# Kernel tuning notes

Hardware: AMD Instinct MI355X
Metric: run time of the kernel (lower is better)

The kernel has to match this reference:

```python
import jax, jax.numpy as jnp
import numpy as np

D_IN = 1024
D_OUT = 1024


def setup_inputs() -> dict:
    key = jax.random.key(0)
    kx, kq, kk, kv = jax.random.split(key, 4)
    x = jax.random.normal(kx, (4, 2048, D_IN), dtype=jnp.float32)
    # nn.Linear weight has shape [d_out, d_in]; y = x @ W.T
    s = 1.0 / np.sqrt(D_IN)
    W_query = jax.random.uniform(kq, (D_OUT, D_IN), jnp.float32, -s, s)
    W_key = jax.random.uniform(kk, (D_OUT, D_IN), jnp.float32, -s, s)
    W_value = jax.random.uniform(kv, (D_OUT, D_IN), jnp.float32, -s, s)
    return {"x": x, "W_query": W_query, "W_key": W_key, "W_value": W_value}


def reference(x, W_query, W_key, W_value):
    # x: [b, n, d_in]; W_*: [d_out, d_in]
    q = jnp.einsum("bnd,kd->bnk", x, W_query)
    k = jnp.einsum("bnd,kd->bnk", x, W_key)
    v = jnp.einsum("bnd,kd->bnk", x, W_value)
    d_k = W_query.shape[0]
    scores = jnp.einsum("bqk,bnk->bqn", q, k) * (d_k ** -0.5)  # [b, n, n]
    weights = jax.nn.softmax(scores, axis=-1)
    return jnp.einsum("bqn,bnk->bqk", weights, v)
```

## Files before the change

### kernel.cpp

```cpp
#include <hip/hip_runtime.h>
#include <hip/hip_bf16.h>
#include <stdint.h>


typedef __attribute__((ext_vector_type(8))) short bf16x8;
typedef __attribute__((ext_vector_type(4))) float f32x4;

__device__ __forceinline__ void async_copy16(const void* g, void* l) {
  __builtin_amdgcn_global_load_lds(
      (__attribute__((address_space(1))) void*)(g),
      (__attribute__((address_space(3))) void*)(l),
      16, 0, 0);
}

__global__ __launch_bounds__(256)
void gemm_qkv(const __hip_bfloat16* __restrict__ A,
              const __hip_bfloat16* __restrict__ B,
              __hip_bfloat16* __restrict__ Q,
              __hip_bfloat16* __restrict__ Kk,
              __hip_bfloat16* __restrict__ Vt)
{
  __shared__ __align__(16) __hip_bfloat16 As[128 * 64];
  __shared__ __align__(16) __hip_bfloat16 Bs[128 * 64];

  const int K = 1024;
  const long long tile_m = (long long)blockIdx.y * 128;
  const long long tile_n = (long long)blockIdx.x * 128;

  const int tid  = threadIdx.x;
  const int wid  = tid >> 6;
  const int lane = tid & 63;

  const int srow = wid * 8 + (lane >> 3);
  const int scol = (((lane & 7) ^ (lane >> 3))) * 8;

  const __hip_bfloat16* aptr = A + (tile_m + srow) * K + scol;
  const __hip_bfloat16* bptr = B + (tile_n + srow) * K + scol;
  char* la = (char*)As + (wid * 8) * 128;
  char* lb = (char*)Bs + (wid * 8) * 128;

  const int wm   = (wid >> 1) * 64;
  const int wn   = (wid & 1) * 64;
  const int quad = lane >> 4;
  const int l16  = lane & 15;
  const int sw   = l16 & 7;

  const bf16x8* Asv = (const bf16x8*)As;
  const bf16x8* Bsv = (const bf16x8*)Bs;

  f32x4 acc[4][4];
  #pragma unroll
  for (int mi = 0; mi < 4; ++mi)
    #pragma unroll
    for (int ni = 0; ni < 4; ++ni)
      acc[mi][ni] = (f32x4){0.f, 0.f, 0.f, 0.f};

  for (int k0 = 0; k0 < K; k0 += 64) {
    #pragma unroll
    for (int p = 0; p < 4; ++p) {
      async_copy16(aptr + (long long)p * 32 * K, la + p * 32 * 128);
      async_copy16(bptr + (long long)p * 32 * K, lb + p * 32 * 128);
    }
    aptr += 64;
    bptr += 64;
    __syncthreads();

    #pragma unroll
    for (int kk = 0; kk < 2; ++kk) {
      bf16x8 af[4], bfr[4];
      const int ch = (kk * 4 + quad);
      #pragma unroll
      for (int mi = 0; mi < 4; ++mi) af[mi]  = Asv[(wm + mi * 16 + l16) * 8 + (ch ^ sw)];
      #pragma unroll
      for (int ni = 0; ni < 4; ++ni) bfr[ni] = Bsv[(wn + ni * 16 + l16) * 8 + (ch ^ sw)];
      #pragma unroll
      for (int mi = 0; mi < 4; ++mi)
        #pragma unroll
        for (int ni = 0; ni < 4; ++ni)
          acc[mi][ni] = __builtin_amdgcn_mfma_f32_16x16x32_bf16(af[mi], bfr[ni], acc[mi][ni], 0, 0, 0);
    }
    __syncthreads();
  }

  const int mat = (int)(tile_n >> 10);
  if (mat < 2) {
    __hip_bfloat16* outp = (mat == 0) ? Q : Kk;
    const float scale = (mat == 0) ? 0.03125f : 1.0f;
    const int coln0 = (int)(tile_n & 1023);
    #pragma unroll
    for (int mi = 0; mi < 4; ++mi) {
      #pragma unroll
      for (int r = 0; r < 4; ++r) {
        const long long row = tile_m + wm + mi * 16 + quad * 4 + r;
        #pragma unroll
        for (int ni = 0; ni < 4; ++ni) {
          const int col = coln0 + wn + ni * 16 + l16;
          outp[row * 1024 + col] = __float2bfloat16(acc[mi][ni][r] * scale);
        }
      }
    }
  } else {
    const int b    = (int)(tile_m >> 11);
    const int seq0 = (int)(tile_m & 2047);
    const int d0   = (int)(tile_n - 2048);
    #pragma unroll
    for (int mi = 0; mi < 4; ++mi) {
      const int seq = seq0 + wm + mi * 16 + quad * 4;
      #pragma unroll
      for (int ni = 0; ni < 4; ++ni) {
        const int d = d0 + wn + ni * 16 + l16;
        union { ushort4 u; unsigned short s[4]; } pk;
        #pragma unroll
        for (int r = 0; r < 4; ++r)
          pk.s[r] = __bfloat16_as_ushort(__float2bfloat16(acc[mi][ni][r]));
        *(ushort4*)(Vt + ((long long)(b * 1024 + d)) * 2048 + seq) = pk.u;
      }
    }
  }
}

__global__ __launch_bounds__(256)
void gemm_s_exp(const __hip_bfloat16* __restrict__ A,
                const __hip_bfloat16* __restrict__ B,
                __hip_bfloat16* __restrict__ Cout,
                float* __restrict__ part)
{
  __shared__ __align__(16) __hip_bfloat16 As[128 * 64];
  __shared__ __align__(16) __hip_bfloat16 Bs[128 * 64];

  const int K = 1024, N = 2048;
  const int bz = blockIdx.z;
  A += (long long)bz * 2048 * 1024;
  B += (long long)bz * 2048 * 1024;

  const long long tile_m = (long long)blockIdx.y * 128;
  const long long tile_n = (long long)blockIdx.x * 128;

  const int tid  = threadIdx.x;
  const int wid  = tid >> 6;
  const int lane = tid & 63;

  const int srow = wid * 8 + (lane >> 3);
  const int scol = (((lane & 7) ^ (lane >> 3))) * 8;

  const __hip_bfloat16* aptr = A + (tile_m + srow) * K + scol;
  const __hip_bfloat16* bptr = B + (tile_n + srow) * K + scol;
  char* la = (char*)As + (wid * 8) * 128;
  char* lb = (char*)Bs + (wid * 8) * 128;

  const int wm   = (wid >> 1) * 64;
  const int wn   = (wid & 1) * 64;
  const int quad = lane >> 4;
  const int l16  = lane & 15;
  const int sw   = l16 & 7;

  const bf16x8* Asv = (const bf16x8*)As;
  const bf16x8* Bsv = (const bf16x8*)Bs;

  f32x4 acc[4][4];
  #pragma unroll
  for (int mi = 0; mi < 4; ++mi)
    #pragma unroll
    for (int ni = 0; ni < 4; ++ni)
      acc[mi][ni] = (f32x4){0.f, 0.f, 0.f, 0.f};

  for (int k0 = 0; k0 < K; k0 += 64) {
    #pragma unroll
    for (int p = 0; p < 4; ++p) {
      async_copy16(aptr + (long long)p * 32 * K, la + p * 32 * 128);
      async_copy16(bptr + (long long)p * 32 * K, lb + p * 32 * 128);
    }
    aptr += 64;
    bptr += 64;
    __syncthreads();

    #pragma unroll
    for (int kk = 0; kk < 2; ++kk) {
      bf16x8 af[4], bfr[4];
      const int ch = (kk * 4 + quad);
      #pragma unroll
      for (int mi = 0; mi < 4; ++mi) af[mi]  = Asv[(wm + mi * 16 + l16) * 8 + (ch ^ sw)];
      #pragma unroll
      for (int ni = 0; ni < 4; ++ni) bfr[ni] = Bsv[(wn + ni * 16 + l16) * 8 + (ch ^ sw)];
      #pragma unroll
      for (int mi = 0; mi < 4; ++mi)
        #pragma unroll
        for (int ni = 0; ni < 4; ++ni)
          acc[mi][ni] = __builtin_amdgcn_mfma_f32_16x16x32_bf16(af[mi], bfr[ni], acc[mi][ni], 0, 0, 0);
    }
    __syncthreads();
  }

  __hip_bfloat16* C = Cout + (long long)bz * 2048 * 2048;
  #pragma unroll
  for (int mi = 0; mi < 4; ++mi) {
    #pragma unroll
    for (int r = 0; r < 4; ++r) {
      const long long row = tile_m + wm + mi * 16 + quad * 4 + r;
      float s = 0.f;
      #pragma unroll
      for (int ni = 0; ni < 4; ++ni) {
        const float e = __expf(acc[mi][ni][r]);
        const __hip_bfloat16 h = __float2bfloat16(e);
        C[row * N + tile_n + wn + ni * 16 + l16] = h;
        s += __bfloat162float(h);
      }
      #pragma unroll
      for (int off = 1; off < 16; off <<= 1) s += __shfl_xor(s, off, 64);
      if (l16 == 0)
        part[((long long)bz * 2048 + row) * 32 + blockIdx.x * 2 + (wid & 1)] = s;
    }
  }
}

__global__ __launch_bounds__(256)
void gemm_pv(const __hip_bfloat16* __restrict__ A,
             const __hip_bfloat16* __restrict__ B,
             const float* __restrict__ part,
             float* __restrict__ Cout)
{
  __shared__ __align__(16) __hip_bfloat16 As[128 * 64];
  __shared__ __align__(16) __hip_bfloat16 Bs[64 * 64];
  __shared__ float rinv[128];

  const int K = 2048, N = 1024;
  const int bz = blockIdx.z;
  A += (long long)bz * 2048 * 2048;
  B += (long long)bz * 1024 * 2048;

  const long long tile_m = (long long)blockIdx.y * 128;
  const long long tile_n = (long long)blockIdx.x * 64;

  const int tid  = threadIdx.x;
  const int wid  = tid >> 6;
  const int lane = tid & 63;

  const int srow = wid * 8 + (lane >> 3);
  const int scol = (((lane & 7) ^ (lane >> 3))) * 8;

  const __hip_bfloat16* aptr = A + (tile_m + srow) * K + scol;
  const __hip_bfloat16* bptr = B + (tile_n + srow) * K + scol;
  char* la = (char*)As + (wid * 8) * 128;
  char* lb = (char*)Bs + (wid * 8) * 128;

  const int wm   = (wid >> 1) * 64;
  const int wn   = (wid & 1) * 32;
  const int quad = lane >> 4;
  const int l16  = lane & 15;
  const int sw   = l16 & 7;

  const bf16x8* Asv = (const bf16x8*)As;
  const bf16x8* Bsv = (const bf16x8*)Bs;

  f32x4 acc[4][2];
  #pragma unroll
  for (int mi = 0; mi < 4; ++mi)
    #pragma unroll
    for (int ni = 0; ni < 2; ++ni)
      acc[mi][ni] = (f32x4){0.f, 0.f, 0.f, 0.f};

  for (int k0 = 0; k0 < K; k0 += 64) {
    #pragma unroll
    for (int p = 0; p < 4; ++p)
      async_copy16(aptr + (long long)p * 32 * K, la + p * 32 * 128);
    #pragma unroll
    for (int p = 0; p < 2; ++p)
      async_copy16(bptr + (long long)p * 32 * K, lb + p * 32 * 128);
    aptr += 64;
    bptr += 64;
    __syncthreads();

    #pragma unroll
    for (int kk = 0; kk < 2; ++kk) {
      bf16x8 af[4], bfr[2];
      const int ch = (kk * 4 + quad);
      #pragma unroll
      for (int mi = 0; mi < 4; ++mi) af[mi]  = Asv[(wm + mi * 16 + l16) * 8 + (ch ^ sw)];
      #pragma unroll
      for (int ni = 0; ni < 2; ++ni) bfr[ni] = Bsv[(wn + ni * 16 + l16) * 8 + (ch ^ sw)];
      #pragma unroll
      for (int mi = 0; mi < 4; ++mi)
        #pragma unroll
        for (int ni = 0; ni < 2; ++ni)
          acc[mi][ni] = __builtin_amdgcn_mfma_f32_16x16x32_bf16(af[mi], bfr[ni], acc[mi][ni], 0, 0, 0);
    }
    __syncthreads();
  }

  if (tid < 128) {
    const float4* pp = (const float4*)(part + ((long long)bz * 2048 + tile_m + tid) * 32);
    float s = 0.f;
    #pragma unroll
    for (int j = 0; j < 8; ++j) {
      const float4 f = pp[j];
      s += f.x + f.y + f.z + f.w;
    }
    rinv[tid] = 1.f / s;
  }
  __syncthreads();

  float* C = Cout + (long long)bz * 2048 * 1024;
  #pragma unroll
  for (int mi = 0; mi < 4; ++mi) {
    #pragma unroll
    for (int r = 0; r < 4; ++r) {
      const int rloc = wm + mi * 16 + quad * 4 + r;
      const float inv = rinv[rloc];
      const long long row = tile_m + rloc;
      #pragma unroll
      for (int ni = 0; ni < 2; ++ni) {
        const long long col = tile_n + wn + ni * 16 + l16;
        C[row * N + col] = acc[mi][ni][r] * inv;
      }
    }
  }
}

__global__ __launch_bounds__(256)
void cast_all(const float* __restrict__ x,
              const float* __restrict__ Wq, const float* __restrict__ Wk,
              const float* __restrict__ Wv,
              __hip_bfloat16* __restrict__ xb, __hip_bfloat16* __restrict__ wcat)
{
  const int bx = blockIdx.x;
  const float* src;
  __hip_bfloat16* dst;
  int i;
  if (bx < 8192) {
    src = x; dst = xb; i = bx * 256 + threadIdx.x;
  } else {
    const int which = (bx - 8192) >> 10;
    src = (which == 0) ? Wq : (which == 1) ? Wk : Wv;
    dst = wcat + (long long)which * 1048576;
    i = ((bx - 8192) & 1023) * 256 + threadIdx.x;
  }
  const float4 f = ((const float4*)src)[i];
  union { ushort4 u; __hip_bfloat16 h[4]; } r;
  r.h[0] = __float2bfloat16(f.x);
  r.h[1] = __float2bfloat16(f.y);
  r.h[2] = __float2bfloat16(f.z);
  r.h[3] = __float2bfloat16(f.w);
  ((ushort4*)dst)[i] = r.u;
}

extern "C" void kernel_launch(void* const* d_in, const int* in_sizes, int n_in,
                              void* d_out, int out_size, void* d_ws, size_t ws_size,
                              hipStream_t stream)
{
  (void)in_sizes; (void)n_in; (void)out_size; (void)ws_size;

  const float* x  = (const float*)d_in[0];
  const float* Wq = (const float*)d_in[1];
  const float* Wk = (const float*)d_in[2];
  const float* Wv = (const float*)d_in[3];
  float* out = (float*)d_out;

  char* ws = (char*)d_ws;
  __hip_bfloat16* xb   = (__hip_bfloat16*)(ws);
  float*          part = (float*)(ws);
  __hip_bfloat16* wcat = (__hip_bfloat16*)(ws + (16LL << 20));
  __hip_bfloat16* Q    = (__hip_bfloat16*)(ws + (22LL << 20));
  __hip_bfloat16* Kk   = (__hip_bfloat16*)(ws + (38LL << 20));
  __hip_bfloat16* Vt   = (__hip_bfloat16*)(ws + (54LL << 20));
  __hip_bfloat16* S    = (__hip_bfloat16*)(ws + (70LL << 20));

  cast_all<<<11264, 256, 0, stream>>>(x, Wq, Wk, Wv, xb, wcat);

  gemm_qkv<<<dim3(24, 64, 1), 256, 0, stream>>>(xb, wcat, Q, Kk, Vt);

  gemm_s_exp<<<dim3(16, 16, 4), 256, 0, stream>>>(Q, Kk, S, part);

  gemm_pv<<<dim3(16, 16, 4), 256, 0, stream>>>(S, Vt, part, out);
}
```

Baseline: 250.5 us.

## Fuse cast and three GEMMs into one persistent kernel with grid barriers

Replaces the four separate launches (cast, QKV projection, scores+exp, PV) with one persistent 1024-block kernel. Each phase becomes a device function, and software grid barriers built on atomic counters separate the phases. The aim is to remove the launch gaps and tail idle time between kernels. In exchange it relies on all 1024 blocks being co-resident, caps registers through launch_bounds(256,4), and keeps the barrier counters in the tail of the output buffer; a wrong guess about residency could deadlock, and the register cap could cause spills.

```diff
diff --git a/kernel.cpp b/kernel.cpp
--- a/kernel.cpp
+++ b/kernel.cpp
@@ -13,19 +13,63 @@
       16, 0, 0);
 }
 
-__global__ __launch_bounds__(256)
-void gemm_qkv(const __hip_bfloat16* __restrict__ A,
-              const __hip_bfloat16* __restrict__ B,
-              __hip_bfloat16* __restrict__ Q,
-              __hip_bfloat16* __restrict__ Kk,
-              __hip_bfloat16* __restrict__ Vt)
-{
-  __shared__ __align__(16) __hip_bfloat16 As[128 * 64];
-  __shared__ __align__(16) __hip_bfloat16 Bs[128 * 64];
+__device__ __forceinline__ void grid_barrier(unsigned* cnt, unsigned target) {
+  __syncthreads();
+  if (threadIdx.x == 0) {
+    __threadfence();
+    atomicAdd(cnt, 1u);
+    while (__hip_atomic_load(cnt, __ATOMIC_RELAXED, __HIP_MEMORY_SCOPE_AGENT) < target)
+      __builtin_amdgcn_s_sleep(32);
+    __threadfence();
+  }
+  __syncthreads();
+}
+
+
+__device__ __forceinline__ void phase_cast(
+    const float* __restrict__ x,
+    const float* __restrict__ Wq, const float* __restrict__ Wk,
+    const float* __restrict__ Wv,
+    __hip_bfloat16* __restrict__ xb, __hip_bfloat16* __restrict__ wcat)
+{
+  for (int i = blockIdx.x * 256 + threadIdx.x; i < 2883584; i += 1024 * 256) {
+    const float* src;
+    __hip_bfloat16* dst;
+    int j;
+    if (i < 2097152) {
+      src = x; dst = xb; j = i;
+    } else {
+      const int k = i - 2097152;
+      const int which = k >> 18;
+      src = (which == 0) ? Wq : (which == 1) ? Wk : Wv;
+      dst = wcat + (long long)which * 1048576;
+      j = k & 262143;
+    }
+    const float4 f = ((const float4*)src)[j];
+    union { ushort4 u; __hip_bfloat16 h[4]; } r;
+    r.h[0] = __float2bfloat16(f.x);
+    r.h[1] = __float2bfloat16(f.y);
+    r.h[2] = __float2bfloat16(f.z);
+    r.h[3] = __float2bfloat16(f.w);
+    ((ushort4*)dst)[j] = r.u;
+  }
+}
+
+__device__ __forceinline__ void qkv_tile(
+    char* smem,
+    const __hip_bfloat16* __restrict__ A,
+    const __hip_bfloat16* __restrict__ B,
+    __hip_bfloat16* __restrict__ Q,
+    __hip_bfloat16* __restrict__ Kk,
+    __hip_bfloat16* __restrict__ Vt,
+    int ty, int tx)
+{
+  __hip_bfloat16* As = (__hip_bfloat16*)smem;
+  __hip_bfloat16* Bs = (__hip_bfloat16*)(smem + 16384);
 
   const int K = 1024;
-  const long long tile_m = (long long)blockIdx.y * 128;
-  const long long tile_n = (long long)blockIdx.x * 128;
+  const long long tile_m = (long long)ty * 128;
+  const long long tile_n = (long long)tx * 128;
 
   const int tid  = threadIdx.x;
   const int wid  = tid >> 6;
@@ -119,22 +163,23 @@
   }
 }
 
-__global__ __launch_bounds__(256)
-void gemm_s_exp(const __hip_bfloat16* __restrict__ A,
-                const __hip_bfloat16* __restrict__ B,
-                __hip_bfloat16* __restrict__ Cout,
-                float* __restrict__ part)
-{
-  __shared__ __align__(16) __hip_bfloat16 As[128 * 64];
-  __shared__ __align__(16) __hip_bfloat16 Bs[128 * 64];
+__device__ __forceinline__ void s_exp_tile(
+    char* smem,
+    const __hip_bfloat16* __restrict__ Qg,
+    const __hip_bfloat16* __restrict__ Kg,
+    __hip_bfloat16* __restrict__ Sg,
+    float* __restrict__ part,
+    int bz, int ty, int tx)
+{
+  __hip_bfloat16* As = (__hip_bfloat16*)smem;
+  __hip_bfloat16* Bs = (__hip_bfloat16*)(smem + 16384);
 
   const int K = 1024, N = 2048;
-  const int bz = blockIdx.z;
-  A += (long long)bz * 2048 * 1024;
-  B += (long long)bz * 2048 * 1024;
-
-  const long long tile_m = (long long)blockIdx.y * 128;
-  const long long tile_n = (long long)blockIdx.x * 128;
+  const __hip_bfloat16* A = Qg + (long long)bz * 2048 * 1024;
+  const __hip_bfloat16* B = Kg + (long long)bz * 2048 * 1024;
+
+  const long long tile_m = (long long)ty * 128;
+  const long long tile_n = (long long)tx * 128;
 
   const int tid  = threadIdx.x;
   const int wid  = tid >> 6;
@@ -191,7 +236,7 @@
     __syncthreads();
   }
 
-  __hip_bfloat16* C = Cout + (long long)bz * 2048 * 2048;
+  __hip_bfloat16* C = Sg + (long long)bz * 2048 * 2048;
   #pragma unroll
   for (int mi = 0; mi < 4; ++mi) {
     #pragma unroll
@@ -208,28 +253,29 @@
       #pragma unroll
       for (int off = 1; off < 16; off <<= 1) s += __shfl_xor(s, off, 64);
       if (l16 == 0)
-        part[((long long)bz * 2048 + row) * 32 + blockIdx.x * 2 + (wid & 1)] = s;
-    }
-  }
-}
-
-__global__ __launch_bounds__(256)
-void gemm_pv(const __hip_bfloat16* __restrict__ A,
-             const __hip_bfloat16* __restrict__ B,
-             const float* __restrict__ part,
-             float* __restrict__ Cout)
-{
-  __shared__ __align__(16) __hip_bfloat16 As[128 * 64];
-  __shared__ __align__(16) __hip_bfloat16 Bs[64 * 64];
-  __shared__ float rinv[128];
+        part[((long long)bz * 2048 + row) * 32 + tx * 2 + (wid & 1)] = s;
+    }
+  }
+}
+
+__device__ __forceinline__ void pv_tile(
+    char* smem,
+    const __hip_bfloat16* __restrict__ Sg,
+    const __hip_bfloat16* __restrict__ Vtg,
+    const float* __restrict__ part,
+    float* __restrict__ Cout,
+    int bz, int ty, int tx)
+{
+  __hip_bfloat16* As = (__hip_bfloat16*)smem;
+  __hip_bfloat16* Bs = (__hip_bfloat16*)(smem + 16384);
+  float* rinv = (float*)(smem + 24576);
 
   const int K = 2048, N = 1024;
-  const int bz = blockIdx.z;
-  A += (long long)bz * 2048 * 2048;
-  B += (long long)bz * 1024 * 2048;
-
-  const long long tile_m = (long long)blockIdx.y * 128;
-  const long long tile_n = (long long)blockIdx.x * 64;
+  const __hip_bfloat16* A = Sg  + (long long)bz * 2048 * 2048;
+  const __hip_bfloat16* B = Vtg + (long long)bz * 1024 * 2048;
+
+  const long long tile_m = (long long)ty * 128;
+  const long long tile_n = (long long)tx * 64;
 
   const int tid  = threadIdx.x;
   const int wid  = tid >> 6;
@@ -316,46 +362,17 @@
   }
 }
 
-__global__ __launch_bounds__(256)
-void cast_all(const float* __restrict__ x,
-              const float* __restrict__ Wq, const float* __restrict__ Wk,
+__global__ __launch_bounds__(256, 4)
+void attn_all(const float* __restrict__ x,
+              const float* __restrict__ Wq,
+              const float* __restrict__ Wk,
               const float* __restrict__ Wv,
-              __hip_bfloat16* __restrict__ xb, __hip_bfloat16* __restrict__ wcat)
-{
-  const int bx = blockIdx.x;
-  const float* src;
-  __hip_bfloat16* dst;
-  int i;
-  if (bx < 8192) {
-    src = x; dst = xb; i = bx * 256 + threadIdx.x;
-  } else {
-    const int which = (bx - 8192) >> 10;
-    src = (which == 0) ? Wq : (which == 1) ? Wk : Wv;
-    dst = wcat + (long long)which * 1048576;
-    i = ((bx - 8192) & 1023) * 256 + threadIdx.x;
-  }
-  const float4 f = ((const float4*)src)[i];
-  union { ushort4 u; __hip_bfloat16 h[4]; } r;
-  r.h[0] = __float2bfloat16(f.x);
-  r.h[1] = __float2bfloat16(f.y);
-  r.h[2] = __float2bfloat16(f.z);
-  r.h[3] = __float2bfloat16(f.w);
-  ((ushort4*)dst)[i] = r.u;
-}
-
-extern "C" void kernel_launch(void* const* d_in, const int* in_sizes, int n_in,
-                              void* d_out, int out_size, void* d_ws, size_t ws_size,
-                              hipStream_t stream)
-{
-  (void)in_sizes; (void)n_in; (void)out_size; (void)ws_size;
-
-  const float* x  = (const float*)d_in[0];
-  const float* Wq = (const float*)d_in[1];
-  const float* Wk = (const float*)d_in[2];
-  const float* Wv = (const float*)d_in[3];
-  float* out = (float*)d_out;
-
-  char* ws = (char*)d_ws;
+              float* __restrict__ out,
+              char* __restrict__ ws,
+              unsigned* __restrict__ bar)
+{
+  __shared__ __align__(16) char smem[32768];
+
   __hip_bfloat16* xb   = (__hip_bfloat16*)(ws);
   float*          part = (float*)(ws);
   __hip_bfloat16* wcat = (__hip_bfloat16*)(ws + (16LL << 20));
@@ -364,11 +381,49 @@
   __hip_bfloat16* Vt   = (__hip_bfloat16*)(ws + (54LL << 20));
   __hip_bfloat16* S    = (__hip_bfloat16*)(ws + (70LL << 20));
 
-  cast_all<<<11264, 256, 0, stream>>>(x, Wq, Wk, Wv, xb, wcat);
-
-  gemm_qkv<<<dim3(24, 64, 1), 256, 0, stream>>>(xb, wcat, Q, Kk, Vt);
-
-  gemm_s_exp<<<dim3(16, 16, 4), 256, 0, stream>>>(Q, Kk, S, part);
-
-  gemm_pv<<<dim3(16, 16, 4), 256, 0, stream>>>(S, Vt, part, out);
-}
+  phase_cast(x, Wq, Wk, Wv, xb, wcat);
+  grid_barrier(bar + 0, 1024);
+
+  for (int t = blockIdx.x; t < 1536; t += 1024) {
+    const int tx = t % 24;
+    const int ty = t / 24;
+    qkv_tile(smem, xb, wcat, Q, Kk, Vt, ty, tx);
+  }
+  grid_barrier(bar + 16, 1024);
+
+  {
+    const int t  = blockIdx.x;
+    const int tx = t & 15;
+    const int ty = (t >> 4) & 15;
+    const int bz = t >> 8;
+    s_exp_tile(smem, Q, Kk, S, part, bz, ty, tx);
+  }
+  grid_barrier(bar + 32, 1024);
+
+  {
+    const int t  = blockIdx.x;
+    const int tx = t & 15;
+    const int ty = (t >> 4) & 15;
+    const int bz = t >> 8;
+    pv_tile(smem, S, Vt, part, out, bz, ty, tx);
+  }
+}
+
+extern "C" void kernel_launch(void* const* d_in, const int* in_sizes, int n_in,
+                              void* d_out, int out_size, void* d_ws, size_t ws_size,
+                              hipStream_t stream)
+{
+  (void)in_sizes; (void)n_in; (void)ws_size;
+
+  const float* x  = (const float*)d_in[0];
+  const float* Wq = (const float*)d_in[1];
+  const float* Wk = (const float*)d_in[2];
+  const float* Wv = (const float*)d_in[3];
+  float* out = (float*)d_out;
+  char* ws = (char*)d_ws;
+
+  unsigned* bar = (unsigned*)(out + out_size - 64);
+  hipMemsetAsync(bar, 0, 256, stream);
+
+  attn_all<<<dim3(1024), dim3(256), 0, stream>>>(x, Wq, Wk, Wv, out, ws, bar);
+}
```

Result: slower. 665.2 us (+165.6%).
